# Kernel tuning notes

Measured on AMD Instinct MI355X. Metric: run time of the kernel, lower is better.

## Reference

```python
import jax, jax.numpy as jnp
import numpy as np

WS = 8        # window size (square)
HEADS = 8
DIM = 512
EPS = 1e-5


def _ln(x, g, b):
    m = x.mean(-1, keepdims=True)
    v = x.var(-1, keepdims=True)
    return (x - m) / jnp.sqrt(v + EPS) * g + b


def _bn(x, g, b, m, v):
    # eval-mode BatchNorm2d on NCHW
    sh = (1, -1, 1, 1)
    return (x - m.reshape(sh)) / jnp.sqrt(v.reshape(sh) + EPS) * g.reshape(sh) + b.reshape(sh)


def _win_rev(w, H, W, C):
    # (B*nW, WS*WS, C) -> (B, C, H, W)
    x = w.reshape(-1, H // WS, W // WS, WS, WS, C)
    return x.transpose(0, 5, 1, 3, 2, 4).reshape(-1, C, H, W)


def _win_part(x):
    # (B, C, H, W) -> (B*nW, WS*WS, C)
    B, C, H, W = x.shape
    x = x.reshape(B, C, H // WS, WS, W // WS, WS)
    return x.transpose(0, 2, 4, 3, 5, 1).reshape(-1, WS * WS, C)


def setup_inputs() -> dict:
    key = jax.random.key(0)
    ks = iter(jax.random.split(key, 64))
    def nrm(sh, s=0.02):
        return jax.random.normal(next(ks), sh, jnp.float32) * s
    C, C2, C8 = DIM, DIM // 2, DIM // 8
    B, H, W = 2, 224, 224
    N = WS * WS
    B_ = B * (H // WS) * (W // WS)
    # relative position index (same construction as the torch module)
    coords = np.stack(np.meshgrid(np.arange(WS), np.arange(WS), indexing='ij'))
    cf = coords.reshape(2, -1)
    rel = (cf[:, :, None] - cf[:, None, :]).transpose(1, 2, 0).astype(np.int64)
    rel[:, :, 0] += WS - 1
    rel[:, :, 1] += WS - 1
    rel[:, :, 0] *= 2 * WS - 1
    rel_idx = jnp.asarray(rel.sum(-1), jnp.int32)   # (N, N)
    ones = lambda n: jnp.ones((n,), jnp.float32)
    zeros = lambda n: jnp.zeros((n,), jnp.float32)
    return dict(
        x=jax.random.normal(next(ks), (B_, N, C), jnp.float32),
        w_pa=nrm((C, C2)), b_pa=zeros(C2),
        g_lna=ones(C2) + nrm((C2,), 0.1), b_lna=nrm((C2,), 0.1),
        w_pc=nrm((C, C)), b_pc=zeros(C),
        g_lnc=ones(C) + nrm((C,), 0.1), b_lnc=nrm((C,), 0.1),
        dw_w=nrm((C, 1, 3, 3), 0.1), dw_b=zeros(C),
        g_bn1=ones(C), b_bn1=zeros(C), m_bn1=nrm((C,), 0.1), v_bn1=ones(C),
        ci_w1=nrm((C, C8)), ci_b1=zeros(C8),
        g_bn2=ones(C8), b_bn2=zeros(C8), m_bn2=nrm((C8,), 0.1), v_bn2=ones(C8),
        ci_w2=nrm((C8, C2)), ci_b2=zeros(C2),
        pj_w=nrm((C, C2)), pj_b=zeros(C2),
        g_bn3=ones(C2), b_bn3=zeros(C2), m_bn3=nrm((C2,), 0.1), v_bn3=ones(C2),
        w_qkv=nrm((C2, 3 * C2)), b_qkv=zeros(3 * C2),
        si_w1=nrm((C2, C8)), si_b1=zeros(C8),
        g_bn4=ones(C8), b_bn4=zeros(C8), m_bn4=nrm((C8,), 0.1), v_bn4=ones(C8),
        si_w2=nrm((C8, 1)), si_b2=zeros(1),
        g_lno=ones(C2) + nrm((C2,), 0.1), b_lno=nrm((C2,), 0.1),
        w_out=nrm((C, C)), b_out=zeros(C),
        rpb=nrm(((2 * WS - 1) ** 2, HEADS)),
        rel_idx=rel_idx, H=H, W=W,
    )


def _forward(x, w_pa, b_pa, g_lna, b_lna, w_pc, b_pc, g_lnc, b_lnc,
             dw_w, dw_b, g_bn1, b_bn1, m_bn1, v_bn1,
             ci_w1, ci_b1, g_bn2, b_bn2, m_bn2, v_bn2, ci_w2, ci_b2,
             pj_w, pj_b, g_bn3, b_bn3, m_bn3, v_bn3,
             w_qkv, b_qkv,
             si_w1, si_b1, g_bn4, b_bn4, m_bn4, v_bn4, si_w2, si_b2,
             g_lno, b_lno, w_out, b_out, rpb, rel_idx, H, W):
    B_, N, C = x.shape
    C2 = C // 2
    hd = C2 // HEADS
    scale = hd ** -0.5
    x_att = _ln(x @ w_pa + b_pa, g_lna, b_lna)            # (B_, N, C2)
    x_cnn = _ln(x @ w_pc + b_pc, g_lnc, b_lnc)            # (B_, N, C)
    x_cnn = _win_rev(x_cnn, H, W, C)                      # (B, C, H, W)
    # depthwise 3x3 conv + BN + GELU
    x_cnn = jax.lax.conv_general_dilated(
        x_cnn, dw_w, (1, 1), [(1, 1), (1, 1)],
        feature_group_count=C, dimension_numbers=('NCHW', 'OIHW', 'NCHW')
    ) + dw_b.reshape(1, -1, 1, 1)
    x_cnn = jax.nn.gelu(_bn(x_cnn, g_bn1, b_bn1, m_bn1, v_bn1), approximate=False)
    # channel interaction: global avg pool -> 1x1 conv -> BN -> GELU -> 1x1 conv
    ci = x_cnn.mean((2, 3))                               # (B, C)
    ci = ci @ ci_w1 + ci_b1                               # (B, C/8)
    ci = jax.nn.gelu((ci - m_bn2) / jnp.sqrt(v_bn2 + EPS) * g_bn2 + b_bn2, approximate=False)
    ci = ci @ ci_w2 + ci_b2                               # (B, C2)
    x_cnn = jnp.einsum('bchw,co->bohw', x_cnn, pj_w) + pj_b.reshape(1, -1, 1, 1)  # (B, C2, H, W)
    # windowed multi-head attention
    qkv = (x_att @ w_qkv + b_qkv).reshape(B_, N, 3, HEADS, hd).transpose(2, 0, 3, 1, 4)
    q, k, v = qkv[0], qkv[1], qkv[2]                      # (B_, heads, N, hd)
    B = ci.shape[0]
    gate = jax.nn.sigmoid(ci).reshape(B, 1, HEADS, 1, hd)
    v = (v.reshape(B, -1, HEADS, N, hd) * gate).reshape(B_, HEADS, N, hd)
    attn = jnp.einsum('bhnd,bhmd->bhnm', q * scale, k)    # (B_, heads, N, N)
    bias = rpb[rel_idx[:N, :N].reshape(-1)].reshape(N, N, HEADS).transpose(2, 0, 1)
    attn = jax.nn.softmax(attn + bias[None], axis=-1)
    x_att = jnp.einsum('bhnm,bhmd->bnhd', attn, v).reshape(B_, N, C2)
    # spatial interaction gating of the conv branch
    x_sp = _win_rev(x_att, H, W, C2)                      # (B, C2, H, W)
    si = jnp.einsum('bchw,co->bohw', x_sp, si_w1) + si_b1.reshape(1, -1, 1, 1)
    si = jax.nn.gelu(_bn(si, g_bn4, b_bn4, m_bn4, v_bn4), approximate=False)
    si = jnp.einsum('bchw,co->bohw', si, si_w2) + si_b2.reshape(1, -1, 1, 1)      # (B, 1, H, W)
    x_cnn = _bn(jax.nn.sigmoid(si) * x_cnn, g_bn3, b_bn3, m_bn3, v_bn3)
    x_cnn = _win_part(x_cnn)                              # (B_, N, C2)
    x_att = _ln(x_att, g_lno, b_lno)
    return jnp.concatenate([x_att, x_cnn], axis=-1) @ w_out + b_out


def reference(x, w_pa, b_pa, g_lna, b_lna, w_pc, b_pc, g_lnc, b_lnc,
              dw_w, dw_b, g_bn1, b_bn1, m_bn1, v_bn1,
              ci_w1, ci_b1, g_bn2, b_bn2, m_bn2, v_bn2, ci_w2, ci_b2,
              pj_w, pj_b, g_bn3, b_bn3, m_bn3, v_bn3,
              w_qkv, b_qkv,
              si_w1, si_b1, g_bn4, b_bn4, m_bn4, v_bn4, si_w2, si_b2,
              g_lno, b_lno, w_out, b_out, rpb, rel_idx, H, W):
    return _forward(x, w_pa, b_pa, g_lna, b_lna, w_pc, b_pc, g_lnc, b_lnc,
                    dw_w, dw_b, g_bn1, b_bn1, m_bn1, v_bn1,
                    ci_w1, ci_b1, g_bn2, b_bn2, m_bn2, v_bn2, ci_w2, ci_b2,
                    pj_w, pj_b, g_bn3, b_bn3, m_bn3, v_bn3,
                    w_qkv, b_qkv,
                    si_w1, si_b1, g_bn4, b_bn4, m_bn4, v_bn4, si_w2, si_b2,
                    g_lno, b_lno, w_out, b_out, rpb, rel_idx, H, W)
```

## Files before the change

kernel.cpp:

```cpp
#include <hip/hip_runtime.h>
#include <math.h>

#define EPS 1e-5f
#define MROWS 100352
#define NWIN  1568

typedef __attribute__((ext_vector_type(8))) short bf16x8;
typedef __attribute__((ext_vector_type(4))) float f32x4;

__device__ __forceinline__ unsigned short f2bf(float f) {
  unsigned u = __float_as_uint(f);
  u += 0x7fffu + ((u >> 16) & 1u);
  return (unsigned short)(u >> 16);
}
__device__ __forceinline__ float bf2f(unsigned short s) {
  return __uint_as_float(((unsigned)s) << 16);
}
__device__ __forceinline__ float gelu_exact(float x) {
  return 0.5f * x * (1.f + erff(x * 0.70710678118654752f));
}

#define GLOAD16(gp, lp)                                              \
  __builtin_amdgcn_global_load_lds(                                  \
      (const __attribute__((address_space(1))) void*)(gp),           \
      (__attribute__((address_space(3))) void*)(lp), 16, 0, 0)

__device__ __forceinline__ void stage_half256(
    const unsigned short* __restrict__ base, int r0, int K, int kk,
    unsigned short* lds, int ldsbase, int tid) {
#pragma unroll
  for (int inst = 0; inst < 2; ++inst) {
    int r = inst * 64 + (tid >> 3);
    int cb = ((tid & 7) << 4) ^ ((r & 7) << 4);
    const unsigned short* src = base + (size_t)(r0 + r) * K + kk + (cb >> 1);
    GLOAD16(src, &lds[ldsbase + inst * 4096 + tid * 8]);
  }
}

__device__ __forceinline__ bf16x8 frag_read256(const unsigned short* lds,
                                               int tilebase, int r_t, int cbyte) {
  int off = r_t * 128 + cbyte;
  int phys = off ^ ((r_t & 7) << 4);
  return *(const bf16x8*)&lds[tilebase + (phys >> 1)];
}

template <bool OUTBF>
__global__ __launch_bounds__(512) void gemm256(
    const unsigned short* __restrict__ A, const unsigned short* __restrict__ Bt,
    const float* __restrict__ bias, void* __restrict__ Cout,
    int M, int N, int K) {
  __shared__ unsigned short lds[65536];
  const int tid = threadIdx.x;
  const int lane = tid & 63, wave = tid >> 6;
  const int wr = wave >> 2;
  const int wcn = wave & 3;
  int bx, by;
  {
    const int nwg = gridDim.x * gridDim.y;
    int n = blockIdx.y * gridDim.x + blockIdx.x;
    int w = ((nwg & 7) == 0) ? ((n & 7) * (nwg >> 3) + (n >> 3)) : n;
    by = w / gridDim.x;
    bx = w - by * gridDim.x;
  }
  const int row0 = by * 256, col0 = bx * 256;
  const int rl = lane & 15, qd = lane >> 4;
  f32x4 acc[8][4];
#pragma unroll
  for (int m = 0; m < 8; ++m)
#pragma unroll
    for (int n = 0; n < 4; ++n) acc[m][n] = (f32x4){0.f, 0.f, 0.f, 0.f};

  const int KT = K >> 6;
  stage_half256(A, row0, K, 0, lds, 0, tid);
  stage_half256(A, row0 + 128, K, 0, lds, 8192, tid);
  stage_half256(Bt, col0, K, 0, lds, 16384, tid);
  stage_half256(Bt, col0 + 128, K, 0, lds, 24576, tid);

  for (int kt = 0; kt < KT; ++kt) {
    const int b = kt & 1;
    const int abase = b * 32768, bbase = b * 32768 + 16384;
    const int nb = b ^ 1;
    const int kkn = (kt + 1) << 6;
    const bool last = (kt == KT - 1);
    bf16x8 bfr[4][2];
#pragma unroll
    for (int p = 0; p < 4; ++p) {
      if (!last) {
        if (p == 0)      stage_half256(A, row0, K, kkn, lds, nb * 32768, tid);
        else if (p == 1) stage_half256(A, row0 + 128, K, kkn, lds, nb * 32768 + 8192, tid);
        else if (p == 2) stage_half256(Bt, col0, K, kkn, lds, nb * 32768 + 16384, tid);
        else             stage_half256(Bt, col0 + 128, K, kkn, lds, nb * 32768 + 24576, tid);
      }
      if (p == 0) {
        if (!last) asm volatile("s_waitcnt vmcnt(2)" ::: "memory");
        else       asm volatile("s_waitcnt vmcnt(0)" ::: "memory");
      }
      __builtin_amdgcn_s_barrier();
      __builtin_amdgcn_sched_barrier(0);
      if (p == 0) {
#pragma unroll
        for (int n = 0; n < 4; ++n)
#pragma unroll
          for (int ks = 0; ks < 2; ++ks)
            bfr[n][ks] = frag_read256(lds, bbase, wcn * 64 + n * 16 + rl,
                                      ks * 64 + qd * 16);
      }
      bf16x8 af[2][2];
#pragma unroll
      for (int i = 0; i < 2; ++i)
#pragma unroll
        for (int ks = 0; ks < 2; ++ks)
          af[i][ks] = frag_read256(lds, abase, wr * 128 + (2 * p + i) * 16 + rl,
                                   ks * 64 + qd * 16);
      __builtin_amdgcn_s_setprio(1);
#pragma unroll
      for (int i = 0; i < 2; ++i)
#pragma unroll
        for (int n = 0; n < 4; ++n)
#pragma unroll
          for (int ks = 0; ks < 2; ++ks)
            acc[2 * p + i][n] = __builtin_amdgcn_mfma_f32_16x16x32_bf16(
                af[i][ks], bfr[n][ks], acc[2 * p + i][n], 0, 0, 0);
      __builtin_amdgcn_s_setprio(0);
      __builtin_amdgcn_s_barrier();
    }
  }
  const int crow = qd * 4, ccol = rl;
#pragma unroll
  for (int n = 0; n < 4; ++n) {
    const int gc = col0 + wcn * 64 + n * 16 + ccol;
    const float bz = bias[gc];
#pragma unroll
    for (int m = 0; m < 8; ++m) {
      const int gr0 = row0 + wr * 128 + m * 16 + crow;
#pragma unroll
      for (int r = 0; r < 4; ++r) {
        float val = acc[m][n][r] + bz;
        if constexpr (OUTBF)
          ((unsigned short*)Cout)[(size_t)(gr0 + r) * N + gc] = f2bf(val);
        else
          ((float*)Cout)[(size_t)(gr0 + r) * N + gc] = val;
      }
    }
  }
}

__global__ __launch_bounds__(256) void wt_convert(const float* __restrict__ in,
                                                  unsigned short* __restrict__ out,
                                                  int K, int N) {
  int i = blockIdx.x * 256 + threadIdx.x;
  if (i >= K * N) return;
  int n = i / K, k = i - n * K;
  out[i] = f2bf(in[(size_t)k * N + n]);
}

__global__ __launch_bounds__(256) void pack_bias(const float* __restrict__ b_pa,
                                                 const float* __restrict__ b_pc,
                                                 float* __restrict__ out) {
  int t = blockIdx.x * 256 + threadIdx.x;
  if (t < 256) out[t] = b_pa[t];
  else if (t < 768) out[t] = b_pc[t - 256];
}

__global__ __launch_bounds__(256) void cvt_bf16(const float* __restrict__ in,
                                                unsigned short* __restrict__ out,
                                                int n8) {
  int i = blockIdx.x * 256 + threadIdx.x;
  if (i >= n8) return;
  float4 a = ((const float4*)in)[i * 2];
  float4 b = ((const float4*)in)[i * 2 + 1];
  ((ushort4*)out)[i * 2] = make_ushort4(f2bf(a.x), f2bf(a.y), f2bf(a.z), f2bf(a.w));
  ((ushort4*)out)[i * 2 + 1] = make_ushort4(f2bf(b.x), f2bf(b.y), f2bf(b.z), f2bf(b.w));
}

template <int W>
__global__ __launch_bounds__(256) void ln_rows_bf(
    const unsigned short* __restrict__ in, int istride,
    unsigned short* __restrict__ out,
    const float* __restrict__ g, const float* __restrict__ b) {
  const int row = blockIdx.x * 4 + (threadIdx.x >> 6);
  const int t = threadIdx.x & 63;
  constexpr int NE = W / 64;
  float v[NE];
  const size_t ibase = (size_t)row * istride + t * NE;
  const size_t obase = (size_t)row * W + t * NE;
#pragma unroll
  for (int c4 = 0; c4 < NE / 4; ++c4) {
    ushort4 u = *(const ushort4*)&in[ibase + c4 * 4];
    v[c4 * 4 + 0] = bf2f(u.x); v[c4 * 4 + 1] = bf2f(u.y);
    v[c4 * 4 + 2] = bf2f(u.z); v[c4 * 4 + 3] = bf2f(u.w);
  }
  float s = 0.f, sq = 0.f;
#pragma unroll
  for (int j = 0; j < NE; ++j) { s += v[j]; sq += v[j] * v[j]; }
#pragma unroll
  for (int off = 32; off >= 1; off >>= 1) {
    s += __shfl_xor(s, off);
    sq += __shfl_xor(sq, off);
  }
  const float mean = s * (1.f / W);
  const float var = sq * (1.f / W) - mean * mean;
  const float rstd = rsqrtf(var + EPS);
#pragma unroll
  for (int c4 = 0; c4 < NE / 4; ++c4) {
    int c = t * NE + c4 * 4;
    ushort4 o = make_ushort4(
        f2bf((v[c4 * 4 + 0] - mean) * rstd * g[c + 0] + b[c + 0]),
        f2bf((v[c4 * 4 + 1] - mean) * rstd * g[c + 1] + b[c + 1]),
        f2bf((v[c4 * 4 + 2] - mean) * rstd * g[c + 2] + b[c + 2]),
        f2bf((v[c4 * 4 + 3] - mean) * rstd * g[c + 3] + b[c + 3]));
    *(ushort4*)&out[obase + c4 * 4] = o;
  }
}

__global__ __launch_bounds__(256) void dwconv_bn_gelu(
    const unsigned short* __restrict__ xin, const float* __restrict__ wgt9,
    const float* __restrict__ dwb, const float* __restrict__ g1,
    const float* __restrict__ b1, const float* __restrict__ m1,
    const float* __restrict__ v1, unsigned short* __restrict__ outp,
    float* __restrict__ ci_part) {
  __shared__ unsigned short tile[100 * 128];
  __shared__ float psum[8 * 128];
  const int b_ = blockIdx.x;
  const int b = b_ / 784, win = b_ % 784;
  const int wi = win / 28, wj = win % 28;
  const int h0 = wi * 8 - 1, w0 = wj * 8 - 1;
  const int tid = threadIdx.x;
  const int c4 = (tid & 31) * 4;
  const int pg = tid >> 5;
  for (int chunk = 0; chunk < 4; ++chunk) {
    const int c0 = chunk * 128;
    __syncthreads();
#pragma unroll
    for (int it = 0; it < 7; ++it) {
      int idx = it * 256 + tid;
      if (idx < 1600) {
        int p = idx >> 4;
        int ch8 = (idx & 15) * 8;
        int ph = h0 + p / 10, pw = w0 + p % 10;
        uint4 val = {0u, 0u, 0u, 0u};
        if (ph >= 0 && ph < 224 && pw >= 0 && pw < 224) {
          int bs = b * 784 + (ph >> 3) * 28 + (pw >> 3);
          int n = ((ph & 7) << 3) | (pw & 7);
          val = *(const uint4*)&xin[(size_t)(bs * 64 + n) * 512 + c0 + ch8];
        }
        *(uint4*)&tile[p * 128 + ch8] = val;
      }
    }
    __syncthreads();
    float wreg[9][4];
    float scale[4], shift[4], bias0[4];
#pragma unroll
    for (int j = 0; j < 4; ++j) {
      int cc = c0 + c4 + j;
#pragma unroll
      for (int k = 0; k < 9; ++k) wreg[k][j] = wgt9[cc * 9 + k];
      scale[j] = g1[cc] * rsqrtf(v1[cc] + EPS);
      shift[j] = b1[cc] - m1[cc] * scale[j];
      bias0[j] = dwb[cc];
    }
    float cs0 = 0.f, cs1 = 0.f, cs2 = 0.f, cs3 = 0.f;
    for (int q = 0; q < 8; ++q) {
      const int qq = pg * 8 + q;
      const int r = qq >> 3, cc_ = qq & 7;
      float a0 = bias0[0], a1 = bias0[1], a2 = bias0[2], a3 = bias0[3];
#pragma unroll
      for (int dr = 0; dr < 3; ++dr)
#pragma unroll
        for (int dc = 0; dc < 3; ++dc) {
          ushort4 u = *(const ushort4*)&tile[((r + dr) * 10 + cc_ + dc) * 128 + c4];
          const int k = dr * 3 + dc;
          a0 += bf2f(u.x) * wreg[k][0];
          a1 += bf2f(u.y) * wreg[k][1];
          a2 += bf2f(u.z) * wreg[k][2];
          a3 += bf2f(u.w) * wreg[k][3];
        }
      float g0 = gelu_exact(a0 * scale[0] + shift[0]);
      float g1v = gelu_exact(a1 * scale[1] + shift[1]);
      float g2v = gelu_exact(a2 * scale[2] + shift[2]);
      float g3v = gelu_exact(a3 * scale[3] + shift[3]);
      cs0 += g0; cs1 += g1v; cs2 += g2v; cs3 += g3v;
      *(ushort4*)&outp[(size_t)(b_ * 64 + qq) * 512 + c0 + c4] =
          make_ushort4(f2bf(g0), f2bf(g1v), f2bf(g2v), f2bf(g3v));
    }
    *(float4*)&psum[pg * 128 + c4] = make_float4(cs0, cs1, cs2, cs3);
    __syncthreads();
    if (tid < 128) {
      float s = 0.f;
#pragma unroll
      for (int g = 0; g < 8; ++g) s += psum[g * 128 + tid];
      ci_part[(size_t)b_ * 512 + c0 + tid] = s;
    }
  }
}

__global__ __launch_bounds__(512) void ci_reduce(const float* __restrict__ ci_part,
                                                 float* __restrict__ ci_mean) {
  const int b = blockIdx.x, c = threadIdx.x;
  float s = 0.f;
  for (int w = 0; w < 784; ++w) s += ci_part[(size_t)(b * 784 + w) * 512 + c];
  ci_mean[b * 512 + c] = s * (1.f / 50176.f);
}

__global__ __launch_bounds__(512) void ci_gate(
    const float* __restrict__ ci_mean, const float* __restrict__ w1,
    const float* __restrict__ bi1, const float* __restrict__ g2,
    const float* __restrict__ b2, const float* __restrict__ m2,
    const float* __restrict__ v2, const float* __restrict__ w2,
    const float* __restrict__ bi2, float* __restrict__ gate) {
  __shared__ float cm[1024];
  __shared__ float c1[128];
  const int t = threadIdx.x;
  cm[t] = ci_mean[t];
  cm[t + 512] = ci_mean[t + 512];
  __syncthreads();
  if (t < 128) {
    int b = t >> 6, j = t & 63;
    float acc = bi1[j];
    for (int c = 0; c < 512; ++c) acc += cm[b * 512 + c] * w1[c * 64 + j];
    float sc = g2[j] * rsqrtf(v2[j] + EPS);
    c1[t] = gelu_exact((acc - m2[j]) * sc + b2[j]);
  }
  __syncthreads();
  {
    int b = t >> 8, o = t & 255;
    float acc = bi2[o];
#pragma unroll
    for (int j = 0; j < 64; ++j) acc += c1[b * 64 + j] * w2[j * 256 + o];
    gate[b * 256 + o] = 1.f / (1.f + expf(-acc));
  }
}

__global__ __launch_bounds__(256) void bias_pre(const float* __restrict__ rpb,
                                                const int* __restrict__ rel,
                                                float* __restrict__ biasf) {
  int i = blockIdx.x * 256 + threadIdx.x;
  if (i >= 4096) return;
  int r = rel[i];
#pragma unroll
  for (int h = 0; h < 8; ++h) biasf[h * 4096 + i] = rpb[r * 8 + h];
}

__global__ __launch_bounds__(256) void attn_mfma(
    const unsigned short* __restrict__ qkv,
    const float* __restrict__ gate,
    const float* __restrict__ biasf,
    unsigned short* __restrict__ outp) {
  __shared__ unsigned short lds[4 * (64 * 68 + 32 * 68)];
  const int w = blockIdx.x;
  const int b = w / 784;
  const int tid = threadIdx.x, lane = tid & 63, wave = tid >> 6;
  unsigned short* p_lds = lds + wave * (64 * 68 + 32 * 68);
  unsigned short* vT = p_lds + 64 * 68;
  const int l15 = lane & 15, l4 = lane >> 4;
  const float scale = 0.17677669529663687f;
  for (int hh = 0; hh < 2; ++hh) {
    const int h = wave * 2 + hh;
    {
      const float* gh = &gate[b * 256 + h * 32];
      const size_t vbase = ((size_t)w * 64 + lane) * 768 + 512 + h * 32;
#pragma unroll
      for (int c = 0; c < 4; ++c) {
        uint4 vv = *(const uint4*)&qkv[vbase + c * 8];
        float4 gA = *(const float4*)&gh[c * 8];
        float4 gB = *(const float4*)&gh[c * 8 + 4];
        unsigned vw[4] = {vv.x, vv.y, vv.z, vv.w};
        float gg[8] = {gA.x, gA.y, gA.z, gA.w, gB.x, gB.y, gB.z, gB.w};
#pragma unroll
        for (int j = 0; j < 4; ++j) {
          int d = c * 8 + j * 2;
          vT[(d + 0) * 68 + lane] = f2bf(__uint_as_float(vw[j] << 16) * gg[j * 2]);
          vT[(d + 1) * 68 + lane] =
              f2bf(__uint_as_float(vw[j] & 0xffff0000u) * gg[j * 2 + 1]);
        }
      }
    }
    bf16x8 kf[4], qf[4];
    const size_t qkbase = (size_t)w * 64 * 768 + h * 32 + l4 * 8;
#pragma unroll
    for (int t = 0; t < 4; ++t) {
      kf[t] = *(const bf16x8*)&qkv[qkbase + (size_t)(t * 16 + l15) * 768 + 256];
      qf[t] = *(const bf16x8*)&qkv[qkbase + (size_t)(t * 16 + l15) * 768];
    }
    f32x4 s[4][4];
#pragma unroll
    for (int mt = 0; mt < 4; ++mt)
#pragma unroll
      for (int nt = 0; nt < 4; ++nt) s[mt][nt] = (f32x4){0.f, 0.f, 0.f, 0.f};
#pragma unroll
    for (int mt = 0; mt < 4; ++mt)
#pragma unroll
      for (int nt = 0; nt < 4; ++nt)
        s[mt][nt] = __builtin_amdgcn_mfma_f32_16x16x32_bf16(kf[mt], qf[nt],
                                                            s[mt][nt], 0, 0, 0);
    float inv_s[4];
#pragma unroll
    for (int nt = 0; nt < 4; ++nt) {
      float mx = -1e30f;
#pragma unroll
      for (int mt = 0; mt < 4; ++mt) {
        float4 b4 = *(const float4*)&biasf[(h * 64 + nt * 16 + l15) * 64 +
                                           mt * 16 + l4 * 4];
        s[mt][nt][0] = s[mt][nt][0] * scale + b4.x;
        s[mt][nt][1] = s[mt][nt][1] * scale + b4.y;
        s[mt][nt][2] = s[mt][nt][2] * scale + b4.z;
        s[mt][nt][3] = s[mt][nt][3] * scale + b4.w;
#pragma unroll
        for (int r = 0; r < 4; ++r) mx = fmaxf(mx, s[mt][nt][r]);
      }
      mx = fmaxf(mx, __shfl_xor(mx, 16));
      mx = fmaxf(mx, __shfl_xor(mx, 32));
      float sum = 0.f;
#pragma unroll
      for (int mt = 0; mt < 4; ++mt)
#pragma unroll
        for (int r = 0; r < 4; ++r) {
          float e = __expf(s[mt][nt][r] - mx);
          s[mt][nt][r] = e;
          sum += e;
        }
      sum += __shfl_xor(sum, 16);
      sum += __shfl_xor(sum, 32);
      inv_s[nt] = 1.f / sum;
    }
#pragma unroll
    for (int nt = 0; nt < 4; ++nt)
#pragma unroll
      for (int mt = 0; mt < 4; ++mt) {
        ushort4 pk = make_ushort4(f2bf(s[mt][nt][0] * inv_s[nt]),
                                  f2bf(s[mt][nt][1] * inv_s[nt]),
                                  f2bf(s[mt][nt][2] * inv_s[nt]),
                                  f2bf(s[mt][nt][3] * inv_s[nt]));
        *(ushort4*)&p_lds[(nt * 16 + l15) * 68 + mt * 16 + l4 * 4] = pk;
      }
    f32x4 o[4][2];
#pragma unroll
    for (int i = 0; i < 4; ++i)
#pragma unroll
      for (int dt = 0; dt < 2; ++dt) o[i][dt] = (f32x4){0.f, 0.f, 0.f, 0.f};
#pragma unroll
    for (int ks = 0; ks < 2; ++ks) {
      bf16x8 pa[4], vf[2];
#pragma unroll
      for (int i = 0; i < 4; ++i) {
        const unsigned short* pp = &p_lds[(i * 16 + l15) * 68 + ks * 32 + l4 * 8];
        union { bf16x8 v; ushort4 u[2]; } tmp;
        tmp.u[0] = *(const ushort4*)pp;
        tmp.u[1] = *(const ushort4*)(pp + 4);
        pa[i] = tmp.v;
      }
#pragma unroll
      for (int dt = 0; dt < 2; ++dt) {
        const unsigned short* vp = &vT[(dt * 16 + l15) * 68 + ks * 32 + l4 * 8];
        union { bf16x8 v; ushort4 u[2]; } tmp;
        tmp.u[0] = *(const ushort4*)vp;
        tmp.u[1] = *(const ushort4*)(vp + 4);
        vf[dt] = tmp.v;
      }
#pragma unroll
      for (int i = 0; i < 4; ++i)
#pragma unroll
        for (int dt = 0; dt < 2; ++dt)
          o[i][dt] = __builtin_amdgcn_mfma_f32_16x16x32_bf16(pa[i], vf[dt],
                                                             o[i][dt], 0, 0, 0);
    }
#pragma unroll
    for (int i = 0; i < 4; ++i)
#pragma unroll
      for (int dt = 0; dt < 2; ++dt)
#pragma unroll
        for (int r = 0; r < 4; ++r)
          outp[((size_t)w * 64 + i * 16 + l4 * 4 + r) * 256 + h * 32 +
               dt * 16 + l15] = f2bf(o[i][dt][r]);
  }
}

__global__ __launch_bounds__(256) void si_ln_concat(
    const unsigned short* __restrict__ xatt, const unsigned short* __restrict__ xpj,
    const float* __restrict__ w1, const float* __restrict__ bi1,
    const float* __restrict__ g4, const float* __restrict__ b4v,
    const float* __restrict__ m4, const float* __restrict__ v4,
    const float* __restrict__ w2, const float* __restrict__ bi2,
    const float* __restrict__ g3, const float* __restrict__ b3v,
    const float* __restrict__ m3, const float* __restrict__ v3,
    const float* __restrict__ glno, const float* __restrict__ blno,
    unsigned short* __restrict__ outc) {
  __shared__ float xr[16 * 256];
  __shared__ float s1s[16 * 64];
  __shared__ float sig[16];
  const int t = threadIdx.x;
  const int row0 = blockIdx.x * 16;
#pragma unroll
  for (int i = 0; i < 2; ++i) {
    int idx = i * 256 + t;
    int pr = idx >> 5, pc = (idx & 31) * 8;
    const unsigned short* src = &xatt[(size_t)(row0 + pr) * 256 + pc];
    ushort4 a = *(const ushort4*)src;
    ushort4 c = *(const ushort4*)(src + 4);
    float* dst = &xr[pr * 256 + pc];
    dst[0] = bf2f(a.x); dst[1] = bf2f(a.y); dst[2] = bf2f(a.z); dst[3] = bf2f(a.w);
    dst[4] = bf2f(c.x); dst[5] = bf2f(c.y); dst[6] = bf2f(c.z); dst[7] = bf2f(c.w);
  }
  __syncthreads();
  {
    const int j = t & 63, pg = t >> 6;
    float acc[4];
    const float bj = bi1[j];
#pragma unroll
    for (int i = 0; i < 4; ++i) acc[i] = bj;
    for (int cc = 0; cc < 256; ++cc) {
      float wv = w1[cc * 64 + j];
#pragma unroll
      for (int i = 0; i < 4; ++i) acc[i] += xr[(pg * 4 + i) * 256 + cc] * wv;
    }
    const float sc4 = g4[j] * rsqrtf(v4[j] + EPS);
    const float m4j = m4[j], b4j = b4v[j];
#pragma unroll
    for (int i = 0; i < 4; ++i)
      s1s[(pg * 4 + i) * 64 + j] = gelu_exact((acc[i] - m4j) * sc4 + b4j);
  }
  __syncthreads();
  if (t < 16) {
    float a2 = bi2[0];
#pragma unroll
    for (int jj = 0; jj < 64; ++jj) a2 += s1s[t * 64 + jj] * w2[jj];
    sig[t] = 1.f / (1.f + expf(-a2));
  }
  __syncthreads();
  {
    const int p = t >> 4, l = t & 15;
    float4 v4s[4];
    float s = 0.f, sq = 0.f;
#pragma unroll
    for (int cq = 0; cq < 4; ++cq) {
      float4 x4 = *(const float4*)&xr[p * 256 + cq * 64 + l * 4];
      v4s[cq] = x4;
      s += x4.x + x4.y + x4.z + x4.w;
      sq += x4.x * x4.x + x4.y * x4.y + x4.z * x4.z + x4.w * x4.w;
    }
#pragma unroll
    for (int off = 8; off >= 1; off >>= 1) {
      s += __shfl_xor(s, off);
      sq += __shfl_xor(sq, off);
    }
    const float mean = s * (1.f / 256.f);
    const float var = sq * (1.f / 256.f) - mean * mean;
    const float rstd = rsqrtf(var + EPS);
    const size_t orow = (size_t)(row0 + p) * 512;
#pragma unroll
    for (int cq = 0; cq < 4; ++cq) {
      int c = cq * 64 + l * 4;
      float4 x4 = v4s[cq];
      *(ushort4*)&outc[orow + c] = make_ushort4(
          f2bf((x4.x - mean) * rstd * glno[c + 0] + blno[c + 0]),
          f2bf((x4.y - mean) * rstd * glno[c + 1] + blno[c + 1]),
          f2bf((x4.z - mean) * rstd * glno[c + 2] + blno[c + 2]),
          f2bf((x4.w - mean) * rstd * glno[c + 3] + blno[c + 3]));
    }
    const float sg = sig[p];
#pragma unroll
    for (int cq = 0; cq < 4; ++cq) {
      int c = cq * 64 + l * 4;
      ushort4 pu = *(const ushort4*)&xpj[(size_t)(row0 + p) * 256 + c];
      float px = bf2f(pu.x), py = bf2f(pu.y), pz = bf2f(pu.z), pw = bf2f(pu.w);
      float sc0 = g3[c + 0] * rsqrtf(v3[c + 0] + EPS);
      float sc1 = g3[c + 1] * rsqrtf(v3[c + 1] + EPS);
      float sc2 = g3[c + 2] * rsqrtf(v3[c + 2] + EPS);
      float sc3 = g3[c + 3] * rsqrtf(v3[c + 3] + EPS);
      *(ushort4*)&outc[orow + 256 + c] = make_ushort4(
          f2bf(sg * px * sc0 + (b3v[c + 0] - m3[c + 0] * sc0)),
          f2bf(sg * py * sc1 + (b3v[c + 1] - m3[c + 1] * sc1)),
          f2bf(sg * pz * sc2 + (b3v[c + 2] - m3[c + 2] * sc2)),
          f2bf(sg * pw * sc3 + (b3v[c + 3] - m3[c + 3] * sc3)));
    }
  }
}

extern "C" void kernel_launch(void* const* d_in, const int* in_sizes, int n_in,
                              void* d_out, int out_size, void* d_ws, size_t ws_size,
                              hipStream_t stream) {
  const float* x     = (const float*)d_in[0];
  const float* w_pa  = (const float*)d_in[1];
  const float* b_pa  = (const float*)d_in[2];
  const float* g_lna = (const float*)d_in[3];
  const float* b_lna = (const float*)d_in[4];
  const float* w_pc  = (const float*)d_in[5];
  const float* b_pc  = (const float*)d_in[6];
  const float* g_lnc = (const float*)d_in[7];
  const float* b_lnc = (const float*)d_in[8];
  const float* dw_w  = (const float*)d_in[9];
  const float* dw_b  = (const float*)d_in[10];
  const float* g_bn1 = (const float*)d_in[11];
  const float* b_bn1 = (const float*)d_in[12];
  const float* m_bn1 = (const float*)d_in[13];
  const float* v_bn1 = (const float*)d_in[14];
  const float* ci_w1 = (const float*)d_in[15];
  const float* ci_b1 = (const float*)d_in[16];
  const float* g_bn2 = (const float*)d_in[17];
  const float* b_bn2 = (const float*)d_in[18];
  const float* m_bn2 = (const float*)d_in[19];
  const float* v_bn2 = (const float*)d_in[20];
  const float* ci_w2 = (const float*)d_in[21];
  const float* ci_b2 = (const float*)d_in[22];
  const float* pj_w  = (const float*)d_in[23];
  const float* pj_b  = (const float*)d_in[24];
  const float* g_bn3 = (const float*)d_in[25];
  const float* b_bn3 = (const float*)d_in[26];
  const float* m_bn3 = (const float*)d_in[27];
  const float* v_bn3 = (const float*)d_in[28];
  const float* w_qkv = (const float*)d_in[29];
  const float* b_qkv = (const float*)d_in[30];
  const float* si_w1 = (const float*)d_in[31];
  const float* si_b1 = (const float*)d_in[32];
  const float* g_bn4 = (const float*)d_in[33];
  const float* b_bn4 = (const float*)d_in[34];
  const float* m_bn4 = (const float*)d_in[35];
  const float* v_bn4 = (const float*)d_in[36];
  const float* si_w2 = (const float*)d_in[37];
  const float* si_b2 = (const float*)d_in[38];
  const float* g_lno = (const float*)d_in[39];
  const float* b_lno = (const float*)d_in[40];
  const float* w_out = (const float*)d_in[41];
  const float* b_out = (const float*)d_in[42];
  const float* rpb   = (const float*)d_in[43];
  const int*   rel   = (const int*)d_in[44];

  char* ws = (char*)d_ws;
  unsigned short* G12BF = (unsigned short*)(ws + 0);
  unsigned short* QKVBF = (unsigned short*)(ws + 0);
  unsigned short* A1BF  = (unsigned short*)(ws + 154140672ull);
  unsigned short* ATTBF = (unsigned short*)(ws + 154140672ull);
  unsigned short* C1BF  = (unsigned short*)(ws + 205520896ull);
  unsigned short* CAT   = (unsigned short*)(ws + 205520896ull);
  unsigned short* XBF   = (unsigned short*)(ws + 308281344ull);
  unsigned short* CVBF  = (unsigned short*)(ws + 308281344ull);
  unsigned short* PJBF  = (unsigned short*)(ws + 411041792ull);
  float*          CIP   = (float*)(ws + 462422016ull);
  float*          CIM   = (float*)(ws + 465633280ull);
  float*          GATE  = (float*)(ws + 465637376ull);
  float*          B12   = (float*)(ws + 465639424ull);
  float*          BIASF = (float*)(ws + 465642496ull);
  unsigned short* WT    = (unsigned short*)(ws + 465773568ull);
  unsigned short* WpaT  = WT + 0;
  unsigned short* WpcT  = WT + 131072;
  unsigned short* PjT   = WT + 393216;
  unsigned short* QkvT  = WT + 524288;
  unsigned short* OutT  = WT + 720896;

  const int M = MROWS;
  dim3 b256(256), b512(512);

  wt_convert<<<512, b256, 0, stream>>>(w_pa, WpaT, 512, 256);
  wt_convert<<<1024, b256, 0, stream>>>(w_pc, WpcT, 512, 512);
  wt_convert<<<512, b256, 0, stream>>>(pj_w, PjT, 512, 256);
  wt_convert<<<768, b256, 0, stream>>>(w_qkv, QkvT, 256, 768);
  wt_convert<<<1024, b256, 0, stream>>>(w_out, OutT, 512, 512);
  pack_bias<<<3, b256, 0, stream>>>(b_pa, b_pc, B12);

  cvt_bf16<<<(M * 512 / 8 + 255) / 256, b256, 0, stream>>>(x, XBF, M * 512 / 8);

  gemm256<true><<<dim3(3, M / 256), dim3(512), 0, stream>>>(XBF, WpaT, B12, G12BF,
                                                            M, 768, 512);
  ln_rows_bf<256><<<M / 4, b256, 0, stream>>>(G12BF, 768, A1BF, g_lna, b_lna);
  ln_rows_bf<512><<<M / 4, b256, 0, stream>>>(G12BF + 256, 768, C1BF, g_lnc, b_lnc);

  dwconv_bn_gelu<<<NWIN, b256, 0, stream>>>(C1BF, dw_w, dw_b, g_bn1, b_bn1, m_bn1,
                                            v_bn1, CVBF, CIP);
  ci_reduce<<<2, b512, 0, stream>>>(CIP, CIM);
  ci_gate<<<1, b512, 0, stream>>>(CIM, ci_w1, ci_b1, g_bn2, b_bn2, m_bn2, v_bn2,
                                  ci_w2, ci_b2, GATE);
  bias_pre<<<16, b256, 0, stream>>>(rpb, rel, BIASF);

  gemm256<true><<<dim3(1, M / 256), dim3(512), 0, stream>>>(CVBF, PjT, pj_b, PJBF,
                                                            M, 256, 512);

  gemm256<true><<<dim3(3, M / 256), dim3(512), 0, stream>>>(A1BF, QkvT, b_qkv, QKVBF,
                                                            M, 768, 256);

  attn_mfma<<<NWIN, b256, 0, stream>>>(QKVBF, GATE, BIASF, ATTBF);

  si_ln_concat<<<M / 16, b256, 0, stream>>>(ATTBF, PJBF, si_w1, si_b1, g_bn4, b_bn4,
                                            m_bn4, v_bn4, si_w2, si_b2, g_bn3,
                                            b_bn3, m_bn3, v_bn3, g_lno, b_lno, CAT);

  gemm256<false><<<dim3(2, M / 256), dim3(512), 0, stream>>>(CAT, OutT, b_out,
                                                             (float*)d_out, M, 512, 512);
}
```

Measured before the change: 843.2 us.

## Fuse attention with spatial-interaction/LN/concat and read fp32 input directly in first GEMM

Merges the attention kernel with the spatial-interaction, layernorm and concat kernel. Each window's attention output now stays in LDS, and the 256-to-64 projection runs on MFMA using a pre-transposed bf16 weight, so the attention output buffer is no longer written and re-read from global memory. The first GEMM now loads fp32 x directly and converts it to bf16 in registers before the LDS write, which removes the separate full-tensor cvt_bf16 pass. Weight, bias and bias-table prep kernels are folded into one launch. The risks are extra register and LDS pressure in the fused kernel and a manually scheduled A pipeline in the new GEMM.

```diff
diff --git a/kernel.cpp b/kernel.cpp
--- a/kernel.cpp
+++ b/kernel.cpp
@@ -52,8 +52,7 @@
   __shared__ unsigned short lds[65536];
   const int tid = threadIdx.x;
   const int lane = tid & 63, wave = tid >> 6;
-  const int wr = wave >> 2;
-  const int wcn = wave & 3;
+  const int wr = wave >> 2, wcn = wave & 3;
   int bx, by;
   {
     const int nwg = gridDim.x * gridDim.y;
@@ -145,32 +144,182 @@
   }
 }
 
-__global__ __launch_bounds__(256) void wt_convert(const float* __restrict__ in,
-                                                  unsigned short* __restrict__ out,
-                                                  int K, int N) {
-  int i = blockIdx.x * 256 + threadIdx.x;
-  if (i >= K * N) return;
-  int n = i / K, k = i - n * K;
-  out[i] = f2bf(in[(size_t)k * N + n]);
-}
-
-__global__ __launch_bounds__(256) void pack_bias(const float* __restrict__ b_pa,
-                                                 const float* __restrict__ b_pc,
-                                                 float* __restrict__ out) {
-  int t = blockIdx.x * 256 + threadIdx.x;
-  if (t < 256) out[t] = b_pa[t];
-  else if (t < 768) out[t] = b_pc[t - 256];
-}
-
-__global__ __launch_bounds__(256) void cvt_bf16(const float* __restrict__ in,
-                                                unsigned short* __restrict__ out,
-                                                int n8) {
-  int i = blockIdx.x * 256 + threadIdx.x;
-  if (i >= n8) return;
-  float4 a = ((const float4*)in)[i * 2];
-  float4 b = ((const float4*)in)[i * 2 + 1];
-  ((ushort4*)out)[i * 2] = make_ushort4(f2bf(a.x), f2bf(a.y), f2bf(a.z), f2bf(a.w));
-  ((ushort4*)out)[i * 2 + 1] = make_ushort4(f2bf(b.x), f2bf(b.y), f2bf(b.z), f2bf(b.w));
+__global__ __launch_bounds__(512, 2) void gemm256_f32a(
+    const float* __restrict__ A, const unsigned short* __restrict__ Bt,
+    const float* __restrict__ bias, unsigned short* __restrict__ Cout,
+    int M, int N, int K) {
+  __shared__ unsigned short lds[65536];
+  const int tid = threadIdx.x;
+  const int lane = tid & 63, wave = tid >> 6;
+  const int wr = wave >> 2, wcn = wave & 3;
+  int bx, by;
+  {
+    const int nwg = gridDim.x * gridDim.y;
+    int n = blockIdx.y * gridDim.x + blockIdx.x;
+    int w = ((nwg & 7) == 0) ? ((n & 7) * (nwg >> 3) + (n >> 3)) : n;
+    by = w / gridDim.x;
+    bx = w - by * gridDim.x;
+  }
+  const int row0 = by * 256, col0 = bx * 256;
+  const int rl = lane & 15, qd = lane >> 4;
+  const int arow = tid >> 2;
+  const int acg = (tid & 3) << 4;
+  f32x4 acc[8][4];
+#pragma unroll
+  for (int m = 0; m < 8; ++m)
+#pragma unroll
+    for (int n = 0; n < 4; ++n) acc[m][n] = (f32x4){0.f, 0.f, 0.f, 0.f};
+
+#define LOADA_F32(st, h, kk)                                                   \
+  {                                                                            \
+    const float* ap = &A[(size_t)(row0 + (h)*128 + arow) * K + (kk) + acg];    \
+    st[0] = *(const float4*)(ap);      st[1] = *(const float4*)(ap + 4);       \
+    st[2] = *(const float4*)(ap + 8);  st[3] = *(const float4*)(ap + 12);      \
+  }
+#define WRITEA_BF(st, base)                                                    \
+  {                                                                            \
+    unsigned q0, q1, q2, q3, q4, q5, q6, q7;                                   \
+    asm("v_cvt_pk_bf16_f32 %0, %1, %2" : "=v"(q0) : "v"(st[0].x), "v"(st[0].y)); \
+    asm("v_cvt_pk_bf16_f32 %0, %1, %2" : "=v"(q1) : "v"(st[0].z), "v"(st[0].w)); \
+    asm("v_cvt_pk_bf16_f32 %0, %1, %2" : "=v"(q2) : "v"(st[1].x), "v"(st[1].y)); \
+    asm("v_cvt_pk_bf16_f32 %0, %1, %2" : "=v"(q3) : "v"(st[1].z), "v"(st[1].w)); \
+    asm("v_cvt_pk_bf16_f32 %0, %1, %2" : "=v"(q4) : "v"(st[2].x), "v"(st[2].y)); \
+    asm("v_cvt_pk_bf16_f32 %0, %1, %2" : "=v"(q5) : "v"(st[2].z), "v"(st[2].w)); \
+    asm("v_cvt_pk_bf16_f32 %0, %1, %2" : "=v"(q6) : "v"(st[3].x), "v"(st[3].y)); \
+    asm("v_cvt_pk_bf16_f32 %0, %1, %2" : "=v"(q7) : "v"(st[3].z), "v"(st[3].w)); \
+    const int sw = (arow & 7) << 4;                                            \
+    const int c0 = ((acg << 1)) ^ sw, c1 = ((acg << 1) + 16) ^ sw;             \
+    *(uint4*)&lds[(base) + ((arow * 128 + c0) >> 1)] = make_uint4(q0, q1, q2, q3); \
+    *(uint4*)&lds[(base) + ((arow * 128 + c1) >> 1)] = make_uint4(q4, q5, q6, q7); \
+  }
+
+  const int KT = K >> 6;
+  {
+    float4 pA0[4], pA1[4];
+    LOADA_F32(pA0, 0, 0);
+    LOADA_F32(pA1, 1, 0);
+    stage_half256(Bt, col0, K, 0, lds, 16384, tid);
+    stage_half256(Bt, col0 + 128, K, 0, lds, 24576, tid);
+    asm volatile("s_waitcnt vmcnt(4)" ::: "memory");
+    WRITEA_BF(pA0, 0);
+    WRITEA_BF(pA1, 8192);
+    asm volatile("s_waitcnt lgkmcnt(0)" ::: "memory");
+  }
+  float4 stA0[4], stA1[4];
+  for (int kt = 0; kt < KT; ++kt) {
+    const int b = kt & 1;
+    const int abase = b * 32768, bbase = b * 32768 + 16384;
+    const int nb = b ^ 1;
+    const int kkn = (kt + 1) << 6;
+    const bool last = (kt == KT - 1);
+    bf16x8 bfr[4][2];
+#pragma unroll
+    for (int p = 0; p < 4; ++p) {
+      if (p == 0) {
+        if (!last) {
+          LOADA_F32(stA0, 0, kkn);
+          asm volatile("s_waitcnt vmcnt(4)" ::: "memory");
+        } else {
+          asm volatile("s_waitcnt vmcnt(0)" ::: "memory");
+        }
+      } else if (p == 1) {
+        if (!last) LOADA_F32(stA1, 1, kkn);
+      } else if (p == 2) {
+        if (!last) {
+          stage_half256(Bt, col0, K, kkn, lds, nb * 32768 + 16384, tid);
+          asm volatile("s_waitcnt vmcnt(6)" ::: "memory");
+          WRITEA_BF(stA0, nb * 32768);
+        }
+      } else {
+        if (!last) {
+          stage_half256(Bt, col0 + 128, K, kkn, lds, nb * 32768 + 24576, tid);
+          asm volatile("s_waitcnt vmcnt(4)" ::: "memory");
+          WRITEA_BF(stA1, nb * 32768 + 8192);
+          asm volatile("s_waitcnt lgkmcnt(0)" ::: "memory");
+        }
+      }
+      __builtin_amdgcn_s_barrier();
+      __builtin_amdgcn_sched_barrier(0);
+      if (p == 0) {
+#pragma unroll
+        for (int n = 0; n < 4; ++n)
+#pragma unroll
+          for (int ks = 0; ks < 2; ++ks)
+            bfr[n][ks] = frag_read256(lds, bbase, wcn * 64 + n * 16 + rl,
+                                      ks * 64 + qd * 16);
+      }
+      bf16x8 af[2][2];
+#pragma unroll
+      for (int i = 0; i < 2; ++i)
+#pragma unroll
+        for (int ks = 0; ks < 2; ++ks)
+          af[i][ks] = frag_read256(lds, abase, wr * 128 + (2 * p + i) * 16 + rl,
+                                   ks * 64 + qd * 16);
+      __builtin_amdgcn_s_setprio(1);
+#pragma unroll
+      for (int i = 0; i < 2; ++i)
+#pragma unroll
+        for (int n = 0; n < 4; ++n)
+#pragma unroll
+          for (int ks = 0; ks < 2; ++ks)
+            acc[2 * p + i][n] = __builtin_amdgcn_mfma_f32_16x16x32_bf16(
+                af[i][ks], bfr[n][ks], acc[2 * p + i][n], 0, 0, 0);
+      __builtin_amdgcn_s_setprio(0);
+      __builtin_amdgcn_s_barrier();
+    }
+  }
+#undef LOADA_F32
+#undef WRITEA_BF
+  const int crow = qd * 4, ccol = rl;
+#pragma unroll
+  for (int n = 0; n < 4; ++n) {
+    const int gc = col0 + wcn * 64 + n * 16 + ccol;
+    const float bz = bias[gc];
+#pragma unroll
+    for (int m = 0; m < 8; ++m) {
+      const int gr0 = row0 + wr * 128 + m * 16 + crow;
+#pragma unroll
+      for (int r = 0; r < 4; ++r)
+        Cout[(size_t)(gr0 + r) * N + gc] = f2bf(acc[m][n][r] + bz);
+    }
+  }
+}
+
+__device__ __forceinline__ void wtc(const float* in, unsigned short* out,
+                                    int K, int N, int i) {
+  if (i < K * N) {
+    int n = i / K, k = i - n * K;
+    out[i] = f2bf(in[(size_t)k * N + n]);
+  }
+}
+
+__global__ __launch_bounds__(256) void prep_all(
+    const float* __restrict__ w_pa, const float* __restrict__ w_pc,
+    const float* __restrict__ pj_w, const float* __restrict__ w_qkv,
+    const float* __restrict__ w_out, const float* __restrict__ si_w1,
+    const float* __restrict__ b_pa, const float* __restrict__ b_pc,
+    const float* __restrict__ rpb, const int* __restrict__ rel,
+    unsigned short* __restrict__ WpaT, unsigned short* __restrict__ WpcT,
+    unsigned short* __restrict__ PjT, unsigned short* __restrict__ QkvT,
+    unsigned short* __restrict__ OutT, unsigned short* __restrict__ SiT,
+    float* __restrict__ B12, float* __restrict__ biasf) {
+  const int blk = blockIdx.x, t = threadIdx.x;
+  if (blk < 512)        wtc(w_pa, WpaT, 512, 256, blk * 256 + t);
+  else if (blk < 1536)  wtc(w_pc, WpcT, 512, 512, (blk - 512) * 256 + t);
+  else if (blk < 2048)  wtc(pj_w, PjT, 512, 256, (blk - 1536) * 256 + t);
+  else if (blk < 2816)  wtc(w_qkv, QkvT, 256, 768, (blk - 2048) * 256 + t);
+  else if (blk < 3840)  wtc(w_out, OutT, 512, 512, (blk - 2816) * 256 + t);
+  else if (blk < 3904)  wtc(si_w1, SiT, 256, 64, (blk - 3840) * 256 + t);
+  else if (blk == 3904) { B12[t] = b_pa[t]; }
+  else if (blk < 3907)  { int i = (blk - 3905) * 256 + t; if (i < 512) B12[256 + i] = b_pc[i]; }
+  else {
+    int i = (blk - 3907) * 256 + t;
+    if (i < 4096) {
+      int r = rel[i];
+#pragma unroll
+      for (int h = 0; h < 8; ++h) biasf[h * 4096 + i] = rpb[r * 8 + h];
+    }
+  }
 }
 
 template <int W>
@@ -331,29 +480,30 @@
   }
 }
 
-__global__ __launch_bounds__(256) void bias_pre(const float* __restrict__ rpb,
-                                                const int* __restrict__ rel,
-                                                float* __restrict__ biasf) {
-  int i = blockIdx.x * 256 + threadIdx.x;
-  if (i >= 4096) return;
-  int r = rel[i];
-#pragma unroll
-  for (int h = 0; h < 8; ++h) biasf[h * 4096 + i] = rpb[r * 8 + h];
-}
-
-__global__ __launch_bounds__(256) void attn_mfma(
+__global__ __launch_bounds__(256) void attn_si(
     const unsigned short* __restrict__ qkv,
-    const float* __restrict__ gate,
-    const float* __restrict__ biasf,
-    unsigned short* __restrict__ outp) {
-  __shared__ unsigned short lds[4 * (64 * 68 + 32 * 68)];
+    const unsigned short* __restrict__ xpj,
+    const float* __restrict__ gate, const float* __restrict__ biasf,
+    const unsigned short* __restrict__ siw1t,
+    const float* __restrict__ bi1, const float* __restrict__ g4,
+    const float* __restrict__ b4v, const float* __restrict__ m4,
+    const float* __restrict__ v4, const float* __restrict__ w2,
+    const float* __restrict__ bi2,
+    const float* __restrict__ g3, const float* __restrict__ b3v,
+    const float* __restrict__ m3, const float* __restrict__ v3,
+    const float* __restrict__ glno, const float* __restrict__ blno,
+    unsigned short* __restrict__ outc) {
+  __shared__ unsigned short smem[26112];
+  __shared__ float sig[64];
   const int w = blockIdx.x;
   const int b = w / 784;
   const int tid = threadIdx.x, lane = tid & 63, wave = tid >> 6;
-  unsigned short* p_lds = lds + wave * (64 * 68 + 32 * 68);
+  unsigned short* p_lds = smem + wave * (64 * 68 + 32 * 68);
   unsigned short* vT = p_lds + 64 * 68;
   const int l15 = lane & 15, l4 = lane >> 4;
   const float scale = 0.17677669529663687f;
+  f32x4 o0[4][2], o1[4][2];
+#pragma unroll
   for (int hh = 0; hh < 2; ++hh) {
     const int h = wave * 2 + hh;
     {
@@ -433,11 +583,11 @@
                                   f2bf(s[mt][nt][3] * inv_s[nt]));
         *(ushort4*)&p_lds[(nt * 16 + l15) * 68 + mt * 16 + l4 * 4] = pk;
       }
-    f32x4 o[4][2];
 #pragma unroll
     for (int i = 0; i < 4; ++i)
 #pragma unroll
-      for (int dt = 0; dt < 2; ++dt) o[i][dt] = (f32x4){0.f, 0.f, 0.f, 0.f};
+      for (int dt = 0; dt < 2; ++dt)
+        (hh ? o1 : o0)[i][dt] = (f32x4){0.f, 0.f, 0.f, 0.f};
 #pragma unroll
     for (int ks = 0; ks < 2; ++ks) {
       bf16x8 pa[4], vf[2];
@@ -461,117 +611,95 @@
       for (int i = 0; i < 4; ++i)
 #pragma unroll
         for (int dt = 0; dt < 2; ++dt)
-          o[i][dt] = __builtin_amdgcn_mfma_f32_16x16x32_bf16(pa[i], vf[dt],
-                                                             o[i][dt], 0, 0, 0);
-    }
+          (hh ? o1 : o0)[i][dt] = __builtin_amdgcn_mfma_f32_16x16x32_bf16(
+              pa[i], vf[dt], (hh ? o1 : o0)[i][dt], 0, 0, 0);
+    }
+  }
+  __syncthreads();
+  unsigned short* xattO = smem;
+#pragma unroll
+  for (int hh = 0; hh < 2; ++hh) {
+    const int h = wave * 2 + hh;
 #pragma unroll
     for (int i = 0; i < 4; ++i)
 #pragma unroll
       for (int dt = 0; dt < 2; ++dt)
 #pragma unroll
         for (int r = 0; r < 4; ++r)
-          outp[((size_t)w * 64 + i * 16 + l4 * 4 + r) * 256 + h * 32 +
-               dt * 16 + l15] = f2bf(o[i][dt][r]);
-  }
-}
-
-__global__ __launch_bounds__(256) void si_ln_concat(
-    const unsigned short* __restrict__ xatt, const unsigned short* __restrict__ xpj,
-    const float* __restrict__ w1, const float* __restrict__ bi1,
-    const float* __restrict__ g4, const float* __restrict__ b4v,
-    const float* __restrict__ m4, const float* __restrict__ v4,
-    const float* __restrict__ w2, const float* __restrict__ bi2,
-    const float* __restrict__ g3, const float* __restrict__ b3v,
-    const float* __restrict__ m3, const float* __restrict__ v3,
-    const float* __restrict__ glno, const float* __restrict__ blno,
-    unsigned short* __restrict__ outc) {
-  __shared__ float xr[16 * 256];
-  __shared__ float s1s[16 * 64];
-  __shared__ float sig[16];
-  const int t = threadIdx.x;
-  const int row0 = blockIdx.x * 16;
-#pragma unroll
-  for (int i = 0; i < 2; ++i) {
-    int idx = i * 256 + t;
-    int pr = idx >> 5, pc = (idx & 31) * 8;
-    const unsigned short* src = &xatt[(size_t)(row0 + pr) * 256 + pc];
-    ushort4 a = *(const ushort4*)src;
-    ushort4 c = *(const ushort4*)(src + 4);
-    float* dst = &xr[pr * 256 + pc];
-    dst[0] = bf2f(a.x); dst[1] = bf2f(a.y); dst[2] = bf2f(a.z); dst[3] = bf2f(a.w);
-    dst[4] = bf2f(c.x); dst[5] = bf2f(c.y); dst[6] = bf2f(c.z); dst[7] = bf2f(c.w);
+          xattO[(i * 16 + l4 * 4 + r) * 264 + h * 32 + dt * 16 + l15] =
+              f2bf((hh ? o1 : o0)[i][dt][r]);
+  }
+  __syncthreads();
+  float* s1s = (float*)(smem + 16896);
+  {
+    f32x4 a4[4];
+#pragma unroll
+    for (int n = 0; n < 4; ++n) a4[n] = (f32x4){0.f, 0.f, 0.f, 0.f};
+#pragma unroll
+    for (int ks = 0; ks < 8; ++ks) {
+      bf16x8 af = *(const bf16x8*)&xattO[(wave * 16 + l15) * 264 + ks * 32 + l4 * 8];
+#pragma unroll
+      for (int n = 0; n < 4; ++n) {
+        bf16x8 bfr = *(const bf16x8*)&siw1t[(n * 16 + l15) * 256 + ks * 32 + l4 * 8];
+        a4[n] = __builtin_amdgcn_mfma_f32_16x16x32_bf16(af, bfr, a4[n], 0, 0, 0);
+      }
+    }
+#pragma unroll
+    for (int n = 0; n < 4; ++n) {
+      const int j = n * 16 + l15;
+      const float sc4 = g4[j] * rsqrtf(v4[j] + EPS);
+      const float m4j = m4[j], b4j = b4v[j], bij = bi1[j];
+#pragma unroll
+      for (int r = 0; r < 4; ++r) {
+        float val = (a4[n][r] + bij - m4j) * sc4 + b4j;
+        s1s[(wave * 16 + l4 * 4 + r) * 68 + j] = gelu_exact(val);
+      }
+    }
+  }
+  __syncthreads();
+  if (tid < 64) {
+    float a2 = bi2[0];
+#pragma unroll
+    for (int jj = 0; jj < 64; ++jj) a2 += s1s[tid * 68 + jj] * w2[jj];
+    sig[tid] = 1.f / (1.f + expf(-a2));
   }
   __syncthreads();
   {
-    const int j = t & 63, pg = t >> 6;
-    float acc[4];
-    const float bj = bi1[j];
-#pragma unroll
-    for (int i = 0; i < 4; ++i) acc[i] = bj;
-    for (int cc = 0; cc < 256; ++cc) {
-      float wv = w1[cc * 64 + j];
-#pragma unroll
-      for (int i = 0; i < 4; ++i) acc[i] += xr[(pg * 4 + i) * 256 + cc] * wv;
-    }
-    const float sc4 = g4[j] * rsqrtf(v4[j] + EPS);
-    const float m4j = m4[j], b4j = b4v[j];
-#pragma unroll
-    for (int i = 0; i < 4; ++i)
-      s1s[(pg * 4 + i) * 64 + j] = gelu_exact((acc[i] - m4j) * sc4 + b4j);
-  }
-  __syncthreads();
-  if (t < 16) {
-    float a2 = bi2[0];
-#pragma unroll
-    for (int jj = 0; jj < 64; ++jj) a2 += s1s[t * 64 + jj] * w2[jj];
-    sig[t] = 1.f / (1.f + expf(-a2));
-  }
-  __syncthreads();
-  {
-    const int p = t >> 4, l = t & 15;
-    float4 v4s[4];
+    const int p = tid >> 2, l = tid & 3;
     float s = 0.f, sq = 0.f;
 #pragma unroll
-    for (int cq = 0; cq < 4; ++cq) {
-      float4 x4 = *(const float4*)&xr[p * 256 + cq * 64 + l * 4];
-      v4s[cq] = x4;
-      s += x4.x + x4.y + x4.z + x4.w;
-      sq += x4.x * x4.x + x4.y * x4.y + x4.z * x4.z + x4.w * x4.w;
-    }
-#pragma unroll
-    for (int off = 8; off >= 1; off >>= 1) {
-      s += __shfl_xor(s, off);
-      sq += __shfl_xor(sq, off);
-    }
+    for (int k = 0; k < 16; ++k) {
+      ushort4 u = *(const ushort4*)&xattO[p * 264 + l * 4 + k * 16];
+      float x0 = bf2f(u.x), x1 = bf2f(u.y), x2 = bf2f(u.z), x3 = bf2f(u.w);
+      s += x0 + x1 + x2 + x3;
+      sq += x0 * x0 + x1 * x1 + x2 * x2 + x3 * x3;
+    }
+    s += __shfl_xor(s, 1);  sq += __shfl_xor(sq, 1);
+    s += __shfl_xor(s, 2);  sq += __shfl_xor(sq, 2);
     const float mean = s * (1.f / 256.f);
     const float var = sq * (1.f / 256.f) - mean * mean;
     const float rstd = rsqrtf(var + EPS);
-    const size_t orow = (size_t)(row0 + p) * 512;
-#pragma unroll
-    for (int cq = 0; cq < 4; ++cq) {
-      int c = cq * 64 + l * 4;
-      float4 x4 = v4s[cq];
+    const size_t orow = ((size_t)w * 64 + p) * 512;
+    const float sg = sig[p];
+#pragma unroll
+    for (int k = 0; k < 16; ++k) {
+      const int c = l * 4 + k * 16;
+      ushort4 u = *(const ushort4*)&xattO[p * 264 + c];
       *(ushort4*)&outc[orow + c] = make_ushort4(
-          f2bf((x4.x - mean) * rstd * glno[c + 0] + blno[c + 0]),
-          f2bf((x4.y - mean) * rstd * glno[c + 1] + blno[c + 1]),
-          f2bf((x4.z - mean) * rstd * glno[c + 2] + blno[c + 2]),
-          f2bf((x4.w - mean) * rstd * glno[c + 3] + blno[c + 3]));
-    }
-    const float sg = sig[p];
-#pragma unroll
-    for (int cq = 0; cq < 4; ++cq) {
-      int c = cq * 64 + l * 4;
-      ushort4 pu = *(const ushort4*)&xpj[(size_t)(row0 + p) * 256 + c];
-      float px = bf2f(pu.x), py = bf2f(pu.y), pz = bf2f(pu.z), pw = bf2f(pu.w);
+          f2bf((bf2f(u.x) - mean) * rstd * glno[c + 0] + blno[c + 0]),
+          f2bf((bf2f(u.y) - mean) * rstd * glno[c + 1] + blno[c + 1]),
+          f2bf((bf2f(u.z) - mean) * rstd * glno[c + 2] + blno[c + 2]),
+          f2bf((bf2f(u.w) - mean) * rstd * glno[c + 3] + blno[c + 3]));
+      ushort4 pu = *(const ushort4*)&xpj[((size_t)w * 64 + p) * 256 + c];
       float sc0 = g3[c + 0] * rsqrtf(v3[c + 0] + EPS);
       float sc1 = g3[c + 1] * rsqrtf(v3[c + 1] + EPS);
       float sc2 = g3[c + 2] * rsqrtf(v3[c + 2] + EPS);
       float sc3 = g3[c + 3] * rsqrtf(v3[c + 3] + EPS);
       *(ushort4*)&outc[orow + 256 + c] = make_ushort4(
-          f2bf(sg * px * sc0 + (b3v[c + 0] - m3[c + 0] * sc0)),
-          f2bf(sg * py * sc1 + (b3v[c + 1] - m3[c + 1] * sc1)),
-          f2bf(sg * pz * sc2 + (b3v[c + 2] - m3[c + 2] * sc2)),
-          f2bf(sg * pw * sc3 + (b3v[c + 3] - m3[c + 3] * sc3)));
+          f2bf(sg * bf2f(pu.x) * sc0 + (b3v[c + 0] - m3[c + 0] * sc0)),
+          f2bf(sg * bf2f(pu.y) * sc1 + (b3v[c + 1] - m3[c + 1] * sc1)),
+          f2bf(sg * bf2f(pu.z) * sc2 + (b3v[c + 2] - m3[c + 2] * sc2)),
+          f2bf(sg * bf2f(pu.w) * sc3 + (b3v[c + 3] - m3[c + 3] * sc3)));
     }
   }
 }
@@ -629,10 +757,8 @@
   unsigned short* G12BF = (unsigned short*)(ws + 0);
   unsigned short* QKVBF = (unsigned short*)(ws + 0);
   unsigned short* A1BF  = (unsigned short*)(ws + 154140672ull);
-  unsigned short* ATTBF = (unsigned short*)(ws + 154140672ull);
   unsigned short* C1BF  = (unsigned short*)(ws + 205520896ull);
   unsigned short* CAT   = (unsigned short*)(ws + 205520896ull);
-  unsigned short* XBF   = (unsigned short*)(ws + 308281344ull);
   unsigned short* CVBF  = (unsigned short*)(ws + 308281344ull);
   unsigned short* PJBF  = (unsigned short*)(ws + 411041792ull);
   float*          CIP   = (float*)(ws + 462422016ull);
@@ -646,21 +772,18 @@
   unsigned short* PjT   = WT + 393216;
   unsigned short* QkvT  = WT + 524288;
   unsigned short* OutT  = WT + 720896;
+  unsigned short* SiT   = WT + 983040;
 
   const int M = MROWS;
   dim3 b256(256), b512(512);
 
-  wt_convert<<<512, b256, 0, stream>>>(w_pa, WpaT, 512, 256);
-  wt_convert<<<1024, b256, 0, stream>>>(w_pc, WpcT, 512, 512);
-  wt_convert<<<512, b256, 0, stream>>>(pj_w, PjT, 512, 256);
-  wt_convert<<<768, b256, 0, stream>>>(w_qkv, QkvT, 256, 768);
-  wt_convert<<<1024, b256, 0, stream>>>(w_out, OutT, 512, 512);
-  pack_bias<<<3, b256, 0, stream>>>(b_pa, b_pc, B12);
-
-  cvt_bf16<<<(M * 512 / 8 + 255) / 256, b256, 0, stream>>>(x, XBF, M * 512 / 8);
-
-  gemm256<true><<<dim3(3, M / 256), dim3(512), 0, stream>>>(XBF, WpaT, B12, G12BF,
-                                                            M, 768, 512);
+  prep_all<<<3923, b256, 0, stream>>>(w_pa, w_pc, pj_w, w_qkv, w_out, si_w1,
+                                      b_pa, b_pc, rpb, rel,
+                                      WpaT, WpcT, PjT, QkvT, OutT, SiT,
+                                      B12, BIASF);
+
+  gemm256_f32a<<<dim3(3, M / 256), dim3(512), 0, stream>>>(x, WpaT, B12, G12BF,
+                                                           M, 768, 512);
   ln_rows_bf<256><<<M / 4, b256, 0, stream>>>(G12BF, 768, A1BF, g_lna, b_lna);
   ln_rows_bf<512><<<M / 4, b256, 0, stream>>>(G12BF + 256, 768, C1BF, g_lnc, b_lnc);
 
@@ -669,7 +792,6 @@
   ci_reduce<<<2, b512, 0, stream>>>(CIP, CIM);
   ci_gate<<<1, b512, 0, stream>>>(CIM, ci_w1, ci_b1, g_bn2, b_bn2, m_bn2, v_bn2,
                                   ci_w2, ci_b2, GATE);
-  bias_pre<<<16, b256, 0, stream>>>(rpb, rel, BIASF);
 
   gemm256<true><<<dim3(1, M / 256), dim3(512), 0, stream>>>(CVBF, PjT, pj_b, PJBF,
                                                             M, 256, 512);
@@ -677,11 +799,11 @@
   gemm256<true><<<dim3(3, M / 256), dim3(512), 0, stream>>>(A1BF, QkvT, b_qkv, QKVBF,
                                                             M, 768, 256);
 
-  attn_mfma<<<NWIN, b256, 0, stream>>>(QKVBF, GATE, BIASF, ATTBF);
-
-  si_ln_concat<<<M / 16, b256, 0, stream>>>(ATTBF, PJBF, si_w1, si_b1, g_bn4, b_bn4,
-                                            m_bn4, v_bn4, si_w2, si_b2, g_bn3,
-                                            b_bn3, m_bn3, v_bn3, g_lno, b_lno, CAT);
+  attn_si<<<NWIN, b256, 0, stream>>>(QKVBF, PJBF, GATE, BIASF, SiT,
+                                     si_b1, g_bn4, b_bn4, m_bn4, v_bn4,
+                                     si_w2, si_b2,
+                                     g_bn3, b_bn3, m_bn3, v_bn3,
+                                     g_lno, b_lno, CAT);
 
   gemm256<false><<<dim3(2, M / 256), dim3(512), 0, stream>>>(CAT, OutT, b_out,
                                                              (float*)d_out, M, 512, 512);
```

After: 929.7 us. 10.3% more time.
